# Optimization experiments

Hardware: AMD Instinct MI355X
Metric: run time of the kernel (lower is better)

The kernel has to match this reference:

```python
import jax, jax.numpy as jnp
import numpy as np
import math

B, N, D_IN, D_H = 8, 2048, 64, 64
PERCENT, KHOP, TAU, EPS = 0.25, 2, 1.0, 1e-10
K_MAX = int(math.ceil(PERCENT * N))  # 512


def setup_inputs() -> dict:
    key = jax.random.key(0)
    ks = jax.random.split(key, 8)
    X = jax.random.normal(ks[0], (B, N, D_IN), dtype=jnp.float32)
    # sparse-ish nonnegative adjacency with self loops (graph-like)
    adj = (jax.random.uniform(ks[1], (B, N, N)) < 0.02).astype(jnp.float32)
    adj = adj + jnp.eye(N, dtype=jnp.float32)[None]
    # variable graph sizes per batch element
    lengths = jnp.array([2048, 1920, 1792, 1664, 1536, 1408, 1280, 1152], dtype=jnp.float32)
    mask = (jnp.arange(N, dtype=jnp.float32)[None, :] < lengths[:, None]).astype(jnp.float32)
    # parameters (xavier-normal-ish for GCN weights)
    s1 = math.sqrt(2.0 / (D_IN + D_H))
    s2 = math.sqrt(2.0 / (D_H + D_H))
    W1 = jax.random.normal(ks[2], (D_IN, D_H), dtype=jnp.float32) * s1
    b1 = jnp.zeros((D_H,), dtype=jnp.float32)
    W2 = jax.random.normal(ks[3], (D_H, D_H), dtype=jnp.float32) * s2
    b2 = jnp.zeros((D_H,), dtype=jnp.float32)
    w_a = jax.random.normal(ks[4], (D_H,), dtype=jnp.float32)
    w_b = jax.random.uniform(ks[5], (D_H,), dtype=jnp.float32, minval=-1.0, maxval=1.0)
    return {"X": X, "adj": adj, "mask": mask, "W1": W1, "b1": b1, "W2": W2, "b2": b2, "w_a": w_a, "w_b": w_b}


def reference(X, adj, mask, W1, b1, W2, b2, w_a, w_b):
    # two GCN layers: y = (adj @ x) @ W + b  (no relu, no residual, no norm)
    h = (adj @ X) @ W1 + b1
    h = (adj @ h) @ W2 + b2
    h = mask[:, :, None] * h                                   # [B,N,H]
    # mean pool over valid nodes
    out = h.sum(axis=1) / (EPS + mask.sum(axis=1, keepdims=True))
    neg = (mask - 1.0) * 1e10
    # att_a computed in original but unused for softmax='neibor'
    att_b = jnp.einsum('bnh,h->bn', h, w_b) + neg
    att_b = jnp.exp((att_b - att_b.max(axis=1, keepdims=True)) * TAU)
    denom = att_b[:, :, None]
    for _ in range(KHOP):
        denom = adj @ denom                                    # khop neighbor aggregation
    att = att_b / (denom[:, :, 0] + EPS)                       # [B,N]
    Z = att[:, :, None] * h                                    # feat_mode='trans'
    # top-k node selection
    k_list = jnp.ceil(PERCENT * mask.sum(axis=1))              # [B]
    _, top_idx = jax.lax.top_k(att, K_MAX)                     # [B,K]
    new_mask = (jnp.arange(K_MAX, dtype=jnp.float32)[None, :] < k_list[:, None]).astype(X.dtype)
    # assignment: gathered adjacency rows, zeroed beyond per-graph k
    assign = jnp.take_along_axis(adj, top_idx[:, :, None], axis=1) * new_mask[:, :, None]  # [B,K,N]
    assign = assign / (assign.sum(axis=1, keepdims=True) + EPS)
    new_adj = jnp.tanh(assign @ adj @ jnp.swapaxes(assign, 1, 2))  # [B,K,K]
    H = assign @ Z                                              # [B,K,H]
    return out, H, new_adj, new_mask
```

## Files before the change

kernel.cpp:

```cpp
#include <hip/hip_runtime.h>

#define BB 8
#define NN 2048
#define DH 64
#define KMAX 512
#define LMAX 128
#define EPSF 1e-10f

__device__ __forceinline__ unsigned f32bits_rn(double x) {
  if (!(x > 0.0)) return 0u;
  float f = (float)x;
  if (f >= 1.17549435e-38f) return __float_as_uint(f);
  double y = x * 0x1p149;
  double r = rint(y);
  unsigned u = (unsigned)r;
  if (u > 0x00800000u) u = 0x00800000u;
  return u;
}

__global__ __launch_bounds__(256) void k_adjlist(
    const float* __restrict__ adj, int* __restrict__ aidx,
    float* __restrict__ aval, int* __restrict__ acnt) {
  const int wave = threadIdx.x >> 6, lane = threadIdx.x & 63;
  const int row = blockIdx.x * 4 + wave;
  const float* arow = adj + (size_t)row * NN;
  int cnt = 0;
  for (int k = 0; k < 32; ++k) cnt += (arow[k * 64 + lane] != 0.f) ? 1 : 0;
  int off = cnt;
  for (int d = 1; d < 64; d <<= 1) {
    int v = __shfl_up(off, d);
    if (lane >= d) off += v;
  }
  const int total = __shfl(off, 63);
  int p = off - cnt;
  int* ai = aidx + (size_t)row * LMAX;
  float* av = aval + (size_t)row * LMAX;
  for (int k = 0; k < 32; ++k) {
    float a = arow[k * 64 + lane];
    if (a != 0.f && p < LMAX) { ai[p] = k * 64 + lane; av[p] = a; ++p; }
  }
  if (lane == 0) acnt[row] = (total < LMAX) ? total : LMAX;
}

__global__ __launch_bounds__(256) void k_layer1(
    const int* __restrict__ aidx, const float* __restrict__ aval,
    const int* __restrict__ acnt, const float* __restrict__ X,
    const float* __restrict__ W, const float* __restrict__ bias,
    float* __restrict__ out) {
  __shared__ float Ws[DH * DH];
  __shared__ float bs[DH];
  for (int t = threadIdx.x; t < DH * DH; t += 256) Ws[t] = W[t];
  if (threadIdx.x < DH) bs[threadIdx.x] = bias[threadIdx.x];
  __syncthreads();
  const int wave = threadIdx.x >> 6, lane = threadIdx.x & 63;
  const int row = blockIdx.x * 4 + wave;
  const int b = row >> 11;
  const float* Xb = X + (size_t)b * NN * DH;
  const int cnt = acnt[row];
  const int* ai = aidx + (size_t)row * LMAX;
  const float* av = aval + (size_t)row * LMAX;
  float acc = 0.f;
  for (int t = 0; t < cnt; ++t)
    acc += av[t] * Xb[(size_t)ai[t] * DH + lane];
  float hv = bs[lane];
  #pragma unroll 8
  for (int k = 0; k < DH; ++k)
    hv += __shfl(acc, k) * Ws[k * DH + lane];
  out[(size_t)row * DH + lane] = hv;
}

__global__ __launch_bounds__(256) void k_layer2(
    const int* __restrict__ aidx, const float* __restrict__ aval,
    const int* __restrict__ acnt, const float* __restrict__ h1,
    const float* __restrict__ W, const float* __restrict__ bias,
    const float* __restrict__ w_b, const float* __restrict__ mask,
    float* __restrict__ h, float* __restrict__ score) {
  __shared__ float Ws[DH * DH];
  __shared__ float bs[DH];
  __shared__ float wbs[DH];
  for (int t = threadIdx.x; t < DH * DH; t += 256) Ws[t] = W[t];
  if (threadIdx.x < DH) { bs[threadIdx.x] = bias[threadIdx.x]; wbs[threadIdx.x] = w_b[threadIdx.x]; }
  __syncthreads();
  const int wave = threadIdx.x >> 6, lane = threadIdx.x & 63;
  const int row = blockIdx.x * 4 + wave;
  const int b = row >> 11, i = row & (NN - 1);
  const float* Hb = h1 + (size_t)b * NN * DH;
  const int cnt = acnt[row];
  const int* ai = aidx + (size_t)row * LMAX;
  const float* av = aval + (size_t)row * LMAX;
  float acc = 0.f;
  for (int t = 0; t < cnt; ++t)
    acc += av[t] * Hb[(size_t)ai[t] * DH + lane];
  float hv = bs[lane];
  #pragma unroll 8
  for (int k = 0; k < DH; ++k)
    hv += __shfl(acc, k) * Ws[k * DH + lane];
  const float m = mask[b * NN + i];
  const float hm = hv * m;
  float sv = hm * wbs[lane];
  for (int off = 32; off; off >>= 1) sv += __shfl_xor(sv, off);
  h[(size_t)row * DH + lane] = hm;
  if (lane == 0) score[b * NN + i] = sv + (m - 1.0f) * 1e10f;
}

__global__ __launch_bounds__(256) void k_out_part(
    const float* __restrict__ h, float* __restrict__ partial) {
  const int b = blockIdx.x >> 5, seg = blockIdx.x & 31;
  const int tid = threadIdx.x, d = tid & 63, g = tid >> 6;
  float s = 0.f;
  for (int i = seg * 64 + g; i < seg * 64 + 64; i += 4)
    s += h[((size_t)b * NN + i) * DH + d];
  __shared__ float red[256];
  red[tid] = s;
  __syncthreads();
  if (g == 0)
    partial[(size_t)blockIdx.x * DH + d] = red[d] + red[d + 64] + red[d + 128] + red[d + 192];
}

__global__ __launch_bounds__(256) void k_out_fin(
    const float* __restrict__ partial, const float* __restrict__ mask,
    float* __restrict__ outp) {
  const int b = blockIdx.x, tid = threadIdx.x;
  float ms = 0.f;
  for (int i = tid; i < NN; i += 256) ms += mask[b * NN + i];
  __shared__ float redm[256];
  redm[tid] = ms;
  __syncthreads();
  for (int st = 128; st > 0; st >>= 1) {
    if (tid < st) redm[tid] += redm[tid + st];
    __syncthreads();
  }
  if (tid < DH) {
    float s = 0.f;
    for (int seg = 0; seg < 32; ++seg)
      s += partial[(size_t)(b * 32 + seg) * DH + tid];
    outp[b * DH + tid] = s / (EPSF + redm[0]);
  }
}

__global__ __launch_bounds__(256) void k_attb(
    const float* __restrict__ score, unsigned* __restrict__ attb_bits,
    float* __restrict__ attb_f) {
  const int b = blockIdx.x, tid = threadIdx.x;
  float mx = -3.4e38f;
  for (int i = tid; i < NN; i += 256) mx = fmaxf(mx, score[b * NN + i]);
  __shared__ float red[256];
  red[tid] = mx;
  __syncthreads();
  for (int st = 128; st > 0; st >>= 1) {
    if (tid < st) red[tid] = fmaxf(red[tid], red[tid + st]);
    __syncthreads();
  }
  const float m = red[0];
  for (int i = tid; i < NN; i += 256) {
    const float dv = (score[b * NN + i] - m) * 1.0f;
    unsigned bits;
    if (dv < -87.3365478515625f) bits = 0u;
    else bits = f32bits_rn(exp((double)dv));
    attb_bits[b * NN + i] = bits;
    attb_f[b * NN + i] = __uint_as_float(bits);
  }
}

__global__ __launch_bounds__(256) void k_matvec(
    const int* __restrict__ aidx, const float* __restrict__ aval,
    const int* __restrict__ acnt, const float* __restrict__ x,
    float* __restrict__ y) {
  __shared__ float xs[NN];
  const int b = (blockIdx.x * 4) >> 11;
  for (int t = threadIdx.x; t < NN; t += 256) xs[t] = x[b * NN + t];
  __syncthreads();
  const int wave = threadIdx.x >> 6, lane = threadIdx.x & 63;
  const int row = blockIdx.x * 4 + wave;
  const int cnt = acnt[row];
  const int* ai = aidx + (size_t)row * LMAX;
  const float* av = aval + (size_t)row * LMAX;
  float s = 0.f;
  for (int t = lane; t < cnt; t += 64) s += av[t] * xs[ai[t]];
  for (int off = 32; off; off >>= 1) s += __shfl_xor(s, off);
  if (lane == 0) y[b * NN + (row & (NN - 1))] = s;
}

__global__ __launch_bounds__(512) void k_topk(
    const unsigned* __restrict__ attb_bits, const float* __restrict__ d2,
    const float* __restrict__ mask, float* __restrict__ att,
    int* __restrict__ topidx, int* __restrict__ klist, float* __restrict__ newmask) {
  __shared__ unsigned key[NN];
  __shared__ int kid[NN];
  __shared__ float redm[512];
  const int b = blockIdx.x, tid = threadIdx.x;
  float ms = 0.f;
  for (int t = tid; t < NN; t += 512) {
    const unsigned ab = attb_bits[b * NN + t];
    const double attd = (double)__uint_as_float(ab);
    const float den = d2[b * NN + t] + 1e-10f;
    const unsigned kb = f32bits_rn(attd / (double)den);
    key[t] = kb; kid[t] = t;
    att[b * NN + t] = __uint_as_float(kb);
    ms += mask[b * NN + t];
  }
  redm[tid] = ms;
  __syncthreads();
  for (int s = 256; s > 0; s >>= 1) {
    if (tid < s) redm[tid] += redm[tid + s];
    __syncthreads();
  }
  const int kl = (int)ceilf(0.25f * redm[0]);
  for (int k = 2; k <= NN; k <<= 1) {
    for (int j = k >> 1; j > 0; j >>= 1) {
      __syncthreads();
      for (int i = tid; i < NN; i += 512) {
        int ixj = i ^ j;
        if (ixj > i) {
          unsigned va = key[i], vb = key[ixj];
          int ia = kid[i], ib = kid[ixj];
          bool a_after_b = (va < vb) || (va == vb && ia > ib);
          bool desc = ((i & k) == 0);
          if (desc ? a_after_b : !a_after_b) {
            key[i] = vb; key[ixj] = va; kid[i] = ib; kid[ixj] = ia;
          }
        }
      }
    }
  }
  __syncthreads();
  for (int r = tid; r < KMAX; r += 512) {
    topidx[b * KMAX + r] = kid[r];
    newmask[b * KMAX + r] = (r < kl) ? 1.0f : 0.0f;
  }
  if (tid == 0) klist[b] = kl;
}

__global__ __launch_bounds__(256) void k_colsum_part(
    const int* __restrict__ aidx, const float* __restrict__ aval,
    const int* __restrict__ acnt, const int* __restrict__ topidx,
    const int* __restrict__ klist, float* __restrict__ scol8) {
  __shared__ float sc[NN];
  const int b = blockIdx.x >> 3, seg = blockIdx.x & 7;
  const int tid = threadIdx.x;
  for (int t = tid; t < NN; t += 256) sc[t] = 0.f;
  __syncthreads();
  const int kl = klist[b];
  const int wave = tid >> 6, lane = tid & 63;
  for (int r = seg + wave * 8; r < kl; r += 32) {
    const int ti = topidx[b * KMAX + r];
    const int c = acnt[b * NN + ti];
    const int* ai = aidx + ((size_t)b * NN + ti) * LMAX;
    const float* av = aval + ((size_t)b * NN + ti) * LMAX;
    for (int s = lane; s < c; s += 64) atomicAdd(&sc[ai[s]], av[s]);
  }
  __syncthreads();
  for (int t = tid; t < NN; t += 256)
    scol8[(size_t)blockIdx.x * NN + t] = sc[t];
}

__global__ __launch_bounds__(256) void k_colsum_merge(
    const float* __restrict__ scol8, float* __restrict__ scol) {
  const int idx = blockIdx.x * 256 + threadIdx.x;
  const int b = idx >> 11, n = idx & (NN - 1);
  float s = 0.f;
  #pragma unroll
  for (int seg = 0; seg < 8; ++seg)
    s += scol8[(size_t)(b * 8 + seg) * NN + n];
  scol[idx] = s;
}

__global__ __launch_bounds__(256) void k_rank_lists(
    const int* __restrict__ aidx, const float* __restrict__ aval,
    const int* __restrict__ acnt, const float* __restrict__ scol,
    const int* __restrict__ topidx, const int* __restrict__ klist,
    int* __restrict__ widxT, float* __restrict__ wvalT, int* __restrict__ rnnz) {
  const int b = blockIdx.x >> 1;
  const int r = (blockIdx.x & 1) * 256 + threadIdx.x;
  const int row = b * KMAX + r;
  int cnt = 0;
  if (r < klist[b]) {
    const int ti = topidx[row];
    cnt = acnt[b * NN + ti];
    const int* ai = aidx + ((size_t)b * NN + ti) * LMAX;
    const float* av = aval + ((size_t)b * NN + ti) * LMAX;
    for (int t = 0; t < cnt; ++t) {
      const int c = ai[t];
      widxT[((size_t)b * LMAX + t) * KMAX + r] = c;
      wvalT[((size_t)b * LMAX + t) * KMAX + r] = av[t] / (scol[b * NN + c] + EPSF);
    }
  }
  rnnz[row] = cnt;
}

__global__ __launch_bounds__(256) void k_M_newadj(
    const int* __restrict__ aidx, const float* __restrict__ aval,
    const int* __restrict__ acnt, const int* __restrict__ widxT,
    const float* __restrict__ wvalT, const int* __restrict__ rnnz,
    float* __restrict__ newadj) {
  const int b = blockIdx.x >> 9, i = blockIdx.x & (KMAX - 1);
  __shared__ float Mrow[NN];
  const int tid = threadIdx.x;
  const int wave = tid >> 6, lane = tid & 63;
  for (int t = tid; t < NN; t += 256) Mrow[t] = 0.f;
  __syncthreads();
  const int nn = rnnz[b * KMAX + i];
  for (int t = wave; t < nn; t += 4) {
    const int k = widxT[((size_t)b * LMAX + t) * KMAX + i];
    const float w = wvalT[((size_t)b * LMAX + t) * KMAX + i];
    const int c = acnt[b * NN + k];
    const int* ai = aidx + ((size_t)b * NN + k) * LMAX;
    const float* av = aval + ((size_t)b * NN + k) * LMAX;
    for (int s = lane; s < c; s += 64) atomicAdd(&Mrow[ai[s]], w * av[s]);
  }
  __syncthreads();
  #pragma unroll
  for (int jj = 0; jj < 2; ++jj) {
    const int j = tid + jj * 256;
    const int nnj = rnnz[b * KMAX + j];
    float a = 0.f;
    for (int t = 0; t < nnj; ++t) {
      const int c = widxT[((size_t)b * LMAX + t) * KMAX + j];
      const float wv = wvalT[((size_t)b * LMAX + t) * KMAX + j];
      a += wv * Mrow[c];
    }
    newadj[((size_t)b * KMAX + i) * KMAX + j] = tanhf(a);
  }
}

__global__ __launch_bounds__(256) void k_H(
    const float* __restrict__ h, const float* __restrict__ att,
    const int* __restrict__ widxT, const float* __restrict__ wvalT,
    const int* __restrict__ rnnz, float* __restrict__ Hout) {
  const int wave = threadIdx.x >> 6, lane = threadIdx.x & 63;
  const int row = blockIdx.x * 4 + wave;
  const int b = row >> 9, r = row & (KMAX - 1);
  const int nn = rnnz[row];
  float acc = 0.f;
  for (int t = 0; t < nn; ++t) {
    const int k = widxT[((size_t)b * LMAX + t) * KMAX + r];
    const float w = wvalT[((size_t)b * LMAX + t) * KMAX + r];
    acc += w * att[b * NN + k] * h[((size_t)b * NN + k) * DH + lane];
  }
  Hout[(size_t)row * DH + lane] = acc;
}

extern "C" void kernel_launch(void* const* d_in, const int* in_sizes, int n_in,
                              void* d_out, int out_size, void* d_ws, size_t ws_size,
                              hipStream_t stream) {
  const float* X    = (const float*)d_in[0];
  const float* adj  = (const float*)d_in[1];
  const float* mask = (const float*)d_in[2];
  const float* W1   = (const float*)d_in[3];
  const float* b1   = (const float*)d_in[4];
  const float* W2   = (const float*)d_in[5];
  const float* b2   = (const float*)d_in[6];
  const float* w_b  = (const float*)d_in[8];

  float* outp    = (float*)d_out;
  float* Hout    = outp + BB * DH;
  float* newadj  = Hout + (size_t)BB * KMAX * DH;
  float* newmask = newadj + (size_t)BB * KMAX * KMAX;

  float* h1 = newadj;

  float* w = (float*)d_ws;
  float* h      = w;                w += (size_t)BB * NN * DH;
  float* score  = w;                w += BB * NN;
  float* attb_f = w;                w += BB * NN;
  float* d1     = w;                w += BB * NN;
  float* d2     = w;                w += BB * NN;
  float* att    = w;                w += BB * NN;
  float* scol   = w;                w += BB * NN;
  float* scol8  = w;                w += (size_t)BB * 8 * NN;
  float* partial= w;                w += (size_t)BB * 32 * DH;
  float* wvalT  = w;                w += (size_t)BB * LMAX * KMAX;
  float* aval   = w;                w += (size_t)BB * NN * LMAX;
  unsigned* attb_bits = (unsigned*)w; w += BB * NN;
  int* aidx    = (int*)w;           w += (size_t)BB * NN * LMAX;
  int* widxT   = (int*)w;           w += (size_t)BB * LMAX * KMAX;
  int* acnt    = (int*)w;           w += BB * NN;
  int* topidx  = (int*)w;           w += BB * KMAX;
  int* rnnz    = (int*)w;           w += BB * KMAX;
  int* klist   = (int*)w;           w += 8;

  k_adjlist<<<BB * NN / 4, 256, 0, stream>>>(adj, aidx, aval, acnt);
  k_layer1<<<BB * NN / 4, 256, 0, stream>>>(aidx, aval, acnt, X, W1, b1, h1);
  k_layer2<<<BB * NN / 4, 256, 0, stream>>>(aidx, aval, acnt, h1, W2, b2, w_b, mask, h, score);
  k_out_part<<<BB * 32, 256, 0, stream>>>(h, partial);
  k_out_fin<<<BB, 256, 0, stream>>>(partial, mask, outp);
  k_attb<<<BB, 256, 0, stream>>>(score, attb_bits, attb_f);
  k_matvec<<<BB * NN / 4, 256, 0, stream>>>(aidx, aval, acnt, attb_f, d1);
  k_matvec<<<BB * NN / 4, 256, 0, stream>>>(aidx, aval, acnt, d1, d2);
  k_topk<<<BB, 512, 0, stream>>>(attb_bits, d2, mask, att, topidx, klist, newmask);
  k_colsum_part<<<BB * 8, 256, 0, stream>>>(aidx, aval, acnt, topidx, klist, scol8);
  k_colsum_merge<<<BB * NN / 256, 256, 0, stream>>>(scol8, scol);
  k_rank_lists<<<BB * 2, 256, 0, stream>>>(aidx, aval, acnt, scol, topidx, klist, widxT, wvalT, rnnz);
  k_M_newadj<<<BB * KMAX, 256, 0, stream>>>(aidx, aval, acnt, widxT, wvalT, rnnz, newadj);
  k_H<<<BB * KMAX / 4, 256, 0, stream>>>(h, att, widxT, wvalT, rnnz, Hout);
}
```

Before: 357.6 us.

## Parallelize softmax, bitonic topk, rank lists, and batch four rows in newadj

Splits the per-batch softmax into a multi-block max pass and an exp pass, giving 64 blocks instead of 8. The bitonic top-k now sorts packed 64-bit keys (value plus reversed index) with 1024 threads, and rank-list building moves from one thread per row to one wave per row. The new_adj kernel computes four M rows per block so each widxT/wvalT column read serves four outputs. The cost is more shared memory per block (32KB for M) and one extra kernel launch.

Measured after the change: 327.9 us. 8.3% less time.

```diff
diff --git a/kernel.cpp b/kernel.cpp
--- a/kernel.cpp
+++ b/kernel.cpp
@@ -6,6 +6,8 @@
 #define KMAX 512
 #define LMAX 128
 #define EPSF 1e-10f
+
+typedef unsigned long long ull;
 
 __device__ __forceinline__ unsigned f32bits_rn(double x) {
   if (!(x > 0.0)) return 0u;
@@ -138,28 +140,35 @@
   }
 }
 
-__global__ __launch_bounds__(256) void k_attb(
-    const float* __restrict__ score, unsigned* __restrict__ attb_bits,
-    float* __restrict__ attb_f) {
-  const int b = blockIdx.x, tid = threadIdx.x;
-  float mx = -3.4e38f;
-  for (int i = tid; i < NN; i += 256) mx = fmaxf(mx, score[b * NN + i]);
+__global__ __launch_bounds__(256) void k_attb_max(
+    const float* __restrict__ score, float* __restrict__ gmaxp) {
+  const int b = blockIdx.x >> 3, seg = blockIdx.x & 7;
+  const int tid = threadIdx.x;
   __shared__ float red[256];
-  red[tid] = mx;
+  red[tid] = score[b * NN + seg * 256 + tid];
   __syncthreads();
   for (int st = 128; st > 0; st >>= 1) {
     if (tid < st) red[tid] = fmaxf(red[tid], red[tid + st]);
     __syncthreads();
   }
-  const float m = red[0];
-  for (int i = tid; i < NN; i += 256) {
-    const float dv = (score[b * NN + i] - m) * 1.0f;
-    unsigned bits;
-    if (dv < -87.3365478515625f) bits = 0u;
-    else bits = f32bits_rn(exp((double)dv));
-    attb_bits[b * NN + i] = bits;
-    attb_f[b * NN + i] = __uint_as_float(bits);
-  }
+  if (tid == 0) gmaxp[blockIdx.x] = red[0];
+}
+
+__global__ __launch_bounds__(256) void k_attb_exp(
+    const float* __restrict__ score, const float* __restrict__ gmaxp,
+    unsigned* __restrict__ attb_bits, float* __restrict__ attb_f) {
+  const int b = blockIdx.x >> 3, seg = blockIdx.x & 7;
+  const int tid = threadIdx.x;
+  float m = gmaxp[b * 8];
+  #pragma unroll
+  for (int s = 1; s < 8; ++s) m = fmaxf(m, gmaxp[b * 8 + s]);
+  const int i = seg * 256 + tid;
+  const float dv = (score[b * NN + i] - m) * 1.0f;
+  unsigned bits;
+  if (dv < -87.3365478515625f) bits = 0u;
+  else bits = f32bits_rn(exp((double)dv));
+  attb_bits[b * NN + i] = bits;
+  attb_f[b * NN + i] = __uint_as_float(bits);
 }
 
 __global__ __launch_bounds__(256) void k_matvec(
@@ -181,27 +190,26 @@
   if (lane == 0) y[b * NN + (row & (NN - 1))] = s;
 }
 
-__global__ __launch_bounds__(512) void k_topk(
+__global__ __launch_bounds__(1024) void k_topk(
     const unsigned* __restrict__ attb_bits, const float* __restrict__ d2,
     const float* __restrict__ mask, float* __restrict__ att,
     int* __restrict__ topidx, int* __restrict__ klist, float* __restrict__ newmask) {
-  __shared__ unsigned key[NN];
-  __shared__ int kid[NN];
-  __shared__ float redm[512];
+  __shared__ ull S[NN];
+  __shared__ float redm[1024];
   const int b = blockIdx.x, tid = threadIdx.x;
   float ms = 0.f;
-  for (int t = tid; t < NN; t += 512) {
+  for (int t = tid; t < NN; t += 1024) {
     const unsigned ab = attb_bits[b * NN + t];
     const double attd = (double)__uint_as_float(ab);
     const float den = d2[b * NN + t] + 1e-10f;
     const unsigned kb = f32bits_rn(attd / (double)den);
-    key[t] = kb; kid[t] = t;
+    S[t] = ((ull)kb << 11) | (ull)(2047 - t);
     att[b * NN + t] = __uint_as_float(kb);
     ms += mask[b * NN + t];
   }
   redm[tid] = ms;
   __syncthreads();
-  for (int s = 256; s > 0; s >>= 1) {
+  for (int s = 512; s > 0; s >>= 1) {
     if (tid < s) redm[tid] += redm[tid + s];
     __syncthreads();
   }
@@ -209,24 +217,21 @@
   for (int k = 2; k <= NN; k <<= 1) {
     for (int j = k >> 1; j > 0; j >>= 1) {
       __syncthreads();
-      for (int i = tid; i < NN; i += 512) {
+      for (int i = tid; i < NN; i += 1024) {
         int ixj = i ^ j;
         if (ixj > i) {
-          unsigned va = key[i], vb = key[ixj];
-          int ia = kid[i], ib = kid[ixj];
-          bool a_after_b = (va < vb) || (va == vb && ia > ib);
-          bool desc = ((i & k) == 0);
-          if (desc ? a_after_b : !a_after_b) {
-            key[i] = vb; key[ixj] = va; kid[i] = ib; kid[ixj] = ia;
-          }
+          const ull pa = S[i], pb = S[ixj];
+          const bool a_after_b = (pa < pb);
+          const bool desc = ((i & k) == 0);
+          if (desc ? a_after_b : !a_after_b) { S[i] = pb; S[ixj] = pa; }
         }
       }
     }
   }
   __syncthreads();
-  for (int r = tid; r < KMAX; r += 512) {
-    topidx[b * KMAX + r] = kid[r];
-    newmask[b * KMAX + r] = (r < kl) ? 1.0f : 0.0f;
+  if (tid < KMAX) {
+    topidx[b * KMAX + tid] = 2047 - (int)(S[tid] & 0x7FFull);
+    newmask[b * KMAX + tid] = (tid < kl) ? 1.0f : 0.0f;
   }
   if (tid == 0) klist[b] = kl;
 }
@@ -270,22 +275,22 @@
     const int* __restrict__ acnt, const float* __restrict__ scol,
     const int* __restrict__ topidx, const int* __restrict__ klist,
     int* __restrict__ widxT, float* __restrict__ wvalT, int* __restrict__ rnnz) {
-  const int b = blockIdx.x >> 1;
-  const int r = (blockIdx.x & 1) * 256 + threadIdx.x;
-  const int row = b * KMAX + r;
+  const int wave = threadIdx.x >> 6, lane = threadIdx.x & 63;
+  const int row = blockIdx.x * 4 + wave;
+  const int b = row >> 9, r = row & (KMAX - 1);
   int cnt = 0;
   if (r < klist[b]) {
     const int ti = topidx[row];
     cnt = acnt[b * NN + ti];
     const int* ai = aidx + ((size_t)b * NN + ti) * LMAX;
     const float* av = aval + ((size_t)b * NN + ti) * LMAX;
-    for (int t = 0; t < cnt; ++t) {
+    for (int t = lane; t < cnt; t += 64) {
       const int c = ai[t];
       widxT[((size_t)b * LMAX + t) * KMAX + r] = c;
       wvalT[((size_t)b * LMAX + t) * KMAX + r] = av[t] / (scol[b * NN + c] + EPSF);
     }
   }
-  rnnz[row] = cnt;
+  if (lane == 0) rnnz[row] = cnt;
 }
 
 __global__ __launch_bounds__(256) void k_M_newadj(
@@ -293,33 +298,43 @@
     const int* __restrict__ acnt, const int* __restrict__ widxT,
     const float* __restrict__ wvalT, const int* __restrict__ rnnz,
     float* __restrict__ newadj) {
-  const int b = blockIdx.x >> 9, i = blockIdx.x & (KMAX - 1);
-  __shared__ float Mrow[NN];
+  const int b = blockIdx.x >> 7, ig = blockIdx.x & 127;
+  const int i0 = ig * 4;
+  __shared__ float Mrow[4][NN];
   const int tid = threadIdx.x;
   const int wave = tid >> 6, lane = tid & 63;
-  for (int t = tid; t < NN; t += 256) Mrow[t] = 0.f;
-  __syncthreads();
-  const int nn = rnnz[b * KMAX + i];
-  for (int t = wave; t < nn; t += 4) {
-    const int k = widxT[((size_t)b * LMAX + t) * KMAX + i];
-    const float w = wvalT[((size_t)b * LMAX + t) * KMAX + i];
-    const int c = acnt[b * NN + k];
-    const int* ai = aidx + ((size_t)b * NN + k) * LMAX;
-    const float* av = aval + ((size_t)b * NN + k) * LMAX;
-    for (int s = lane; s < c; s += 64) atomicAdd(&Mrow[ai[s]], w * av[s]);
+  for (int t = tid; t < 4 * NN; t += 256) ((float*)Mrow)[t] = 0.f;
+  __syncthreads();
+  {
+    const int i = i0 + wave;
+    const int nn = rnnz[b * KMAX + i];
+    for (int t = 0; t < nn; ++t) {
+      const int k = widxT[((size_t)b * LMAX + t) * KMAX + i];
+      const float w = wvalT[((size_t)b * LMAX + t) * KMAX + i];
+      const int c = acnt[b * NN + k];
+      const int* ai = aidx + ((size_t)b * NN + k) * LMAX;
+      const float* av = aval + ((size_t)b * NN + k) * LMAX;
+      for (int s = lane; s < c; s += 64) atomicAdd(&Mrow[wave][ai[s]], w * av[s]);
+    }
   }
   __syncthreads();
   #pragma unroll
   for (int jj = 0; jj < 2; ++jj) {
     const int j = tid + jj * 256;
     const int nnj = rnnz[b * KMAX + j];
-    float a = 0.f;
+    float a0 = 0.f, a1 = 0.f, a2 = 0.f, a3 = 0.f;
     for (int t = 0; t < nnj; ++t) {
       const int c = widxT[((size_t)b * LMAX + t) * KMAX + j];
       const float wv = wvalT[((size_t)b * LMAX + t) * KMAX + j];
-      a += wv * Mrow[c];
+      a0 += wv * Mrow[0][c];
+      a1 += wv * Mrow[1][c];
+      a2 += wv * Mrow[2][c];
+      a3 += wv * Mrow[3][c];
     }
-    newadj[((size_t)b * KMAX + i) * KMAX + j] = tanhf(a);
+    newadj[((size_t)b * KMAX + i0 + 0) * KMAX + j] = tanhf(a0);
+    newadj[((size_t)b * KMAX + i0 + 1) * KMAX + j] = tanhf(a1);
+    newadj[((size_t)b * KMAX + i0 + 2) * KMAX + j] = tanhf(a2);
+    newadj[((size_t)b * KMAX + i0 + 3) * KMAX + j] = tanhf(a3);
   }
 }
 
@@ -369,6 +384,7 @@
   float* scol   = w;                w += BB * NN;
   float* scol8  = w;                w += (size_t)BB * 8 * NN;
   float* partial= w;                w += (size_t)BB * 32 * DH;
+  float* gmaxp  = w;                w += BB * 8;
   float* wvalT  = w;                w += (size_t)BB * LMAX * KMAX;
   float* aval   = w;                w += (size_t)BB * NN * LMAX;
   unsigned* attb_bits = (unsigned*)w; w += BB * NN;
@@ -384,13 +400,14 @@
   k_layer2<<<BB * NN / 4, 256, 0, stream>>>(aidx, aval, acnt, h1, W2, b2, w_b, mask, h, score);
   k_out_part<<<BB * 32, 256, 0, stream>>>(h, partial);
   k_out_fin<<<BB, 256, 0, stream>>>(partial, mask, outp);
-  k_attb<<<BB, 256, 0, stream>>>(score, attb_bits, attb_f);
+  k_attb_max<<<BB * 8, 256, 0, stream>>>(score, gmaxp);
+  k_attb_exp<<<BB * 8, 256, 0, stream>>>(score, gmaxp, attb_bits, attb_f);
   k_matvec<<<BB * NN / 4, 256, 0, stream>>>(aidx, aval, acnt, attb_f, d1);
   k_matvec<<<BB * NN / 4, 256, 0, stream>>>(aidx, aval, acnt, d1, d2);
-  k_topk<<<BB, 512, 0, stream>>>(attb_bits, d2, mask, att, topidx, klist, newmask);
+  k_topk<<<BB, 1024, 0, stream>>>(attb_bits, d2, mask, att, topidx, klist, newmask);
   k_colsum_part<<<BB * 8, 256, 0, stream>>>(aidx, aval, acnt, topidx, klist, scol8);
   k_colsum_merge<<<BB * NN / 256, 256, 0, stream>>>(scol8, scol);
-  k_rank_lists<<<BB * 2, 256, 0, stream>>>(aidx, aval, acnt, scol, topidx, klist, widxT, wvalT, rnnz);
-  k_M_newadj<<<BB * KMAX, 256, 0, stream>>>(aidx, aval, acnt, widxT, wvalT, rnnz, newadj);
+  k_rank_lists<<<BB * KMAX / 4, 256, 0, stream>>>(aidx, aval, acnt, scol, topidx, klist, widxT, wvalT, rnnz);
+  k_M_newadj<<<BB * KMAX / 4, 256, 0, stream>>>(aidx, aval, acnt, widxT, wvalT, rnnz, newadj);
   k_H<<<BB * KMAX / 4, 256, 0, stream>>>(h, att, widxT, wvalT, rnnz, Hout);
 }
```
